# Kernel tuning notes

Measured on AMD Instinct MI355X. Metric: run time of the kernel, lower is better.

## Reference

```python
import jax, jax.numpy as jnp
import numpy as np
from jax import lax

B, A, H, W = 4, 9, 128, 128
FEAT_STRIDE = 16
PRE_NMS_TOPN = 4000
POST_NMS_TOPN = 1000
NMS_THRESH = 0.7
IM_SIZE = 2048.0


def _generate_anchors(base_size=16, ratios=(0.5, 1.0, 2.0), scales=(8.0, 16.0, 32.0)):
    base = np.array([1.0, 1.0, base_size, base_size], dtype=np.float32) - 1.0

    def whctrs(a):
        w = a[2] - a[0] + 1.0
        h = a[3] - a[1] + 1.0
        return w, h, a[0] + 0.5 * (w - 1.0), a[1] + 0.5 * (h - 1.0)

    def mk(ws, hs, xc, yc):
        ws = ws[:, None]
        hs = hs[:, None]
        return np.hstack([xc - 0.5 * (ws - 1.0), yc - 0.5 * (hs - 1.0),
                          xc + 0.5 * (ws - 1.0), yc + 0.5 * (hs - 1.0)])

    w, h, xc, yc = whctrs(base)
    size = w * h
    r = np.array(ratios, dtype=np.float32)
    ws = np.round(np.sqrt(size / r))
    hs = np.round(ws * r)
    ratio_anchors = mk(ws, hs, xc, yc)
    out = []
    s = np.array(scales, dtype=np.float32)
    for a in ratio_anchors:
        w2, h2, xc2, yc2 = whctrs(a)
        out.append(mk(w2 * s, h2 * s, xc2, yc2))
    return np.vstack(out).astype(np.float32)  # [A, 4]


ANCHORS = jnp.asarray(_generate_anchors(FEAT_STRIDE))


def setup_inputs() -> dict:
    key = jax.random.key(0)
    k1, k2 = jax.random.split(key)
    scores = jax.random.normal(k1, (B, 2 * A, H, W), dtype=jnp.float32)
    bbox_deltas = jax.random.normal(k2, (B, 4 * A, H, W), dtype=jnp.float32) * 0.5
    im_info = jnp.tile(jnp.array([IM_SIZE, IM_SIZE, 1.0], dtype=jnp.float32), (B, 1))
    valid_range = jnp.tile(jnp.array([0.0, 10000.0], dtype=jnp.float32), (B, 1))
    return {"scores": scores, "bbox_deltas": bbox_deltas, "im_info": im_info,
            "valid_range": valid_range}


def _bbox_transform_inv(anchors, deltas):
    # anchors [N,4] broadcast against deltas [B,N,4]
    w = anchors[..., 2] - anchors[..., 0] + 1.0
    h = anchors[..., 3] - anchors[..., 1] + 1.0
    cx = anchors[..., 0] + 0.5 * w
    cy = anchors[..., 1] + 0.5 * h
    dx, dy, dw, dh = deltas[..., 0], deltas[..., 1], deltas[..., 2], deltas[..., 3]
    pcx = dx * w + cx
    pcy = dy * h + cy
    pw = jnp.exp(dw) * w
    ph = jnp.exp(dh) * h
    return jnp.stack([pcx - 0.5 * pw, pcy - 0.5 * ph,
                      pcx + 0.5 * pw, pcy + 0.5 * ph], axis=-1)


def _clip_boxes(boxes, im_hw):
    # boxes [B,N,4]; im_hw [B,2] = (height, width)
    boxes = jnp.maximum(boxes, 0.0)
    hmax = im_hw[:, 0][:, None] - 1.0
    wmax = im_hw[:, 1][:, None] - 1.0
    return jnp.stack([jnp.minimum(boxes[..., 0], wmax),
                      jnp.minimum(boxes[..., 1], hmax),
                      jnp.minimum(boxes[..., 2], wmax),
                      jnp.minimum(boxes[..., 3], hmax)], axis=-1)


def _iou_matrix(boxes):
    # boxes [N,4], +1 pixel convention (matches gpu_nms)
    x1, y1, x2, y2 = boxes[:, 0], boxes[:, 1], boxes[:, 2], boxes[:, 3]
    areas = (x2 - x1 + 1.0) * (y2 - y1 + 1.0)
    iw = jnp.maximum(jnp.minimum(x2[:, None], x2[None, :]) - jnp.maximum(x1[:, None], x1[None, :]) + 1.0, 0.0)
    ih = jnp.maximum(jnp.minimum(y2[:, None], y2[None, :]) - jnp.maximum(y1[:, None], y1[None, :]) + 1.0, 0.0)
    inter = iw * ih
    return inter / (areas[:, None] + areas[None, :] - inter)


def _nms_single(proposals, scores_flat):
    # proposals [KA,4], scores_flat [KA] -> [POST,4] zero-padded, score-ordered
    _, order = lax.top_k(scores_flat, PRE_NMS_TOPN)
    boxes = proposals[order]  # [PRE,4] sorted by descending score
    sup_mat = lax.stop_gradient(_iou_matrix(boxes) > NMS_THRESH)
    idxs = jnp.arange(PRE_NMS_TOPN)

    def body(i, supp):
        row = sup_mat[i] & (idxs > i)
        return jnp.where(supp[i], supp, supp | row)

    supp = lax.fori_loop(0, PRE_NMS_TOPN, body, jnp.zeros(PRE_NMS_TOPN, dtype=bool))
    keep = ~supp
    # stable argsort puts kept indices first, preserving score order
    kidx = jnp.argsort(jnp.where(keep, 0, 1), stable=True)[:POST_NMS_TOPN]
    valid = (jnp.arange(POST_NMS_TOPN) < keep.sum()).astype(boxes.dtype)
    return boxes[kidx] * valid[:, None]


def reference(scores, bbox_deltas, im_info, valid_range):
    fg = scores[:, A:, :, :]                      # [B,A,Hf,Wf] objectness scores
    Bc, _, Hf, Wf = fg.shape
    # anchor grid: [K,4] shifts + [A,4] base anchors -> [K*A,4]
    sx = jnp.arange(Wf, dtype=jnp.float32) * FEAT_STRIDE
    sy = jnp.arange(Hf, dtype=jnp.float32) * FEAT_STRIDE
    gx, gy = jnp.meshgrid(sx, sy)                 # [Hf,Wf] (xy indexing like np.meshgrid)
    shifts = jnp.stack([gx.ravel(), gy.ravel(), gx.ravel(), gy.ravel()], axis=1)  # [K,4]
    anchors = (ANCHORS[None, :, :] + shifts[:, None, :]).reshape(-1, 4)           # [K*A,4]

    deltas = bbox_deltas.transpose(0, 2, 3, 1).reshape(Bc, -1, 4)  # [B,K*A,4]
    sc = fg.transpose(0, 2, 3, 1).reshape(Bc, -1)                   # [B,K*A]

    proposals = _bbox_transform_inv(anchors[None, :, :], deltas)
    proposals = _clip_boxes(proposals, im_info[:, :2])

    # filter_proposal_by_range: area = w*h (no +1), score -> -1 if out of range
    widths = proposals[..., 2] - proposals[..., 0]
    heights = proposals[..., 3] - proposals[..., 1]
    area = widths * heights
    min_a = (valid_range[:, 0] ** 2)[:, None]
    max_a = (valid_range[:, 1] ** 2)[:, None]
    sc = jnp.where((area < min_a) | (area > max_a), -1.0, sc)

    out_boxes = jax.vmap(_nms_single)(proposals, sc)  # [B,POST,4]
    batch_col = jnp.broadcast_to(
        jnp.arange(Bc, dtype=out_boxes.dtype)[:, None, None], (Bc, POST_NMS_TOPN, 1))
    return jnp.concatenate([batch_col, out_boxes], axis=-1)  # [B,POST,5]
```

## Files before the change

### kernel.cpp

```cpp
#include <hip/hip_runtime.h>
#include <cmath>

#define WD 128
#define HT 128
#define HW 16384
#define NB 4
#define NA 9
#define NPB (NA*HW)
#define TOPN 4000
#define POSTN 1000
#define CANDCAP 8192
#define MROWS 4096
#define RST 4160
#define NTILE 63
#define TRI (NTILE*(NTILE+1)/2)
#define NREP 4
#define PBLK 576
#define NBLK 42

typedef unsigned long long u64;
typedef unsigned int u32;

struct Anchors { float v[36]; };

static void gen_anchors(float* out) {
    double base[4] = {0.0, 0.0, 15.0, 15.0};
    const double ratios[3] = {0.5, 1.0, 2.0};
    const double scales[3] = {8.0, 16.0, 32.0};
    double w = base[2] - base[0] + 1.0;
    double h = base[3] - base[1] + 1.0;
    double xc = base[0] + 0.5 * (w - 1.0);
    double yc = base[1] + 0.5 * (h - 1.0);
    double size = w * h;
    double ra[3][4];
    for (int r = 0; r < 3; ++r) {
        double ws = nearbyint(sqrt(size / ratios[r]));
        double hs = nearbyint(ws * ratios[r]);
        ra[r][0] = xc - 0.5 * (ws - 1.0);
        ra[r][1] = yc - 0.5 * (hs - 1.0);
        ra[r][2] = xc + 0.5 * (ws - 1.0);
        ra[r][3] = yc + 0.5 * (hs - 1.0);
    }
    int k = 0;
    for (int r = 0; r < 3; ++r) {
        double w2 = ra[r][2] - ra[r][0] + 1.0;
        double h2 = ra[r][3] - ra[r][1] + 1.0;
        double x2c = ra[r][0] + 0.5 * (w2 - 1.0);
        double y2c = ra[r][1] + 0.5 * (h2 - 1.0);
        for (int s = 0; s < 3; ++s) {
            double ws = w2 * scales[s], hs = h2 * scales[s];
            out[k*4+0] = (float)(x2c - 0.5 * (ws - 1.0));
            out[k*4+1] = (float)(y2c - 0.5 * (hs - 1.0));
            out[k*4+2] = (float)(x2c + 0.5 * (ws - 1.0));
            out[k*4+3] = (float)(y2c + 0.5 * (hs - 1.0));
            ++k;
        }
    }
}

__device__ __forceinline__ u32 sortable_key(float sc) {
    u32 sb = __float_as_uint(sc);
    return sb ^ ((sb & 0x80000000u) ? 0xFFFFFFFFu : 0x80000000u);
}

__device__ __forceinline__ u64 readlane64(u64 v, int l) {
    u32 lo = (u32)__builtin_amdgcn_readlane((int)(u32)v, l);
    u32 hi = (u32)__builtin_amdgcn_readlane((int)(u32)(v >> 32), l);
    return ((u64)hi << 32) | lo;
}

__device__ __forceinline__ u64 wave_or64_dpp(u64 v) {
    u32 lo = (u32)v, hi = (u32)(v >> 32);
#define DPPOR(x, ctrl) x |= (u32)__builtin_amdgcn_update_dpp(0, (int)(x), ctrl, 0xf, 0xf, false)
    DPPOR(lo, 0x111); DPPOR(lo, 0x112); DPPOR(lo, 0x114); DPPOR(lo, 0x118);
    DPPOR(lo, 0x142); DPPOR(lo, 0x143);
    DPPOR(hi, 0x111); DPPOR(hi, 0x112); DPPOR(hi, 0x114); DPPOR(hi, 0x118);
    DPPOR(hi, 0x142); DPPOR(hi, 0x143);
#undef DPPOR
    u32 rlo = (u32)__builtin_amdgcn_readlane((int)lo, 63);
    u32 rhi = (u32)__builtin_amdgcn_readlane((int)hi, 63);
    return ((u64)rhi << 32) | rlo;
}

__device__ __forceinline__ float4 decode_box(const float* __restrict__ deltas,
                                             const float* __restrict__ im_info,
                                             const Anchors& A, int b, int a, int p)
{
#pragma clang fp contract(off)
    int hh = p >> 7;
    int ww = p & 127;
    float sx = (float)(ww * 16);
    float sy = (float)(hh * 16);
    float ax1 = A.v[a*4+0] + sx;
    float ay1 = A.v[a*4+1] + sy;
    float ax2 = A.v[a*4+2] + sx;
    float ay2 = A.v[a*4+3] + sy;
    const float* dbase = deltas + ((size_t)(b*36 + a*4))*HW + p;
    float dx = dbase[0];
    float dy = dbase[HW];
    float dw = dbase[2*HW];
    float dh = dbase[3*HW];
    float aw = ax2 - ax1 + 1.0f;
    float ah = ay2 - ay1 + 1.0f;
    float cx = ax1 + 0.5f*aw;
    float cy = ay1 + 0.5f*ah;
    float pcx = dx*aw + cx;
    float pcy = dy*ah + cy;
    float ew = (float)exp((double)dw);
    float eh = (float)exp((double)dh);
    float pw = ew * aw;
    float ph = eh * ah;
    float x1 = pcx - 0.5f*pw;
    float y1 = pcy - 0.5f*ph;
    float x2 = pcx + 0.5f*pw;
    float y2 = pcy + 0.5f*ph;
    float hmax = im_info[b*3+0] - 1.0f;
    float wmax = im_info[b*3+1] - 1.0f;
    x1 = fmaxf(x1, 0.0f); y1 = fmaxf(y1, 0.0f);
    x2 = fmaxf(x2, 0.0f); y2 = fmaxf(y2, 0.0f);
    x1 = fminf(x1, wmax); y1 = fminf(y1, hmax);
    x2 = fminf(x2, wmax); y2 = fminf(y2, hmax);
    return make_float4(x1, y1, x2, y2);
}

__global__ void k_props(const float* __restrict__ scores,
                        const float* __restrict__ deltas,
                        const float* __restrict__ im_info,
                        const float* __restrict__ valid_range,
                        Anchors A,
                        u32* __restrict__ fkeys,
                        u32* __restrict__ coarseH)
{
#pragma clang fp contract(off)
    __shared__ u32 lh[256];
    int tid = threadIdx.x;
    lh[tid] = 0;
    __syncthreads();

    int n = blockIdx.x * 256 + tid;
    int b = n / NPB;
    int r = n - b*NPB;
    int a = r / HW;
    int p = r - a*HW;

    float4 bx = decode_box(deltas, im_info, A, b, a, p);
    float sc = scores[((size_t)(b*18 + 9 + a))*HW + p];
    float area = (bx.z - bx.x) * (bx.w - bx.y);
    float v0 = valid_range[b*2+0], v1 = valid_range[b*2+1];
    if (area < v0*v0 || area > v1*v1) sc = -1.0f;

    u32 key = sortable_key(sc);
    fkeys[n] = key;
    atomicAdd(&lh[key >> 24], 1u);
    __syncthreads();

    u32 v = lh[tid];
    if (v) {
        int rep = blockIdx.x & (NREP-1);
        atomicAdd(&coarseH[((size_t)rep*NB + b)*256 + tid], v);
    }
}

__global__ void k_findA(const u32* __restrict__ coarseH,
                        int* __restrict__ cstar, u32* __restrict__ cabove)
{
    __shared__ u32 sfx[256];
    int b = blockIdx.x, t = threadIdx.x;
    u32 s = 0;
    for (int rr = 0; rr < NREP; ++rr) s += coarseH[((size_t)rr*NB + b)*256 + t];
    sfx[t] = s;
    __syncthreads();
    for (int d = 1; d < 256; d <<= 1) {
        u32 add = (t + d < 256) ? sfx[t + d] : 0u;
        __syncthreads();
        sfx[t] += add;
        __syncthreads();
    }
    u32 mine = sfx[t];
    u32 nxt  = (t < 255) ? sfx[t+1] : 0u;
    if (mine >= TOPN && (t == 255 || nxt < TOPN)) { cstar[b] = t; cabove[b] = nxt; }
}

__global__ void k_fineHist(const u32* __restrict__ fkeys,
                           const int* __restrict__ cstar,
                           u32* __restrict__ fineH)
{
    int n = blockIdx.x * 256 + threadIdx.x;
    int b = n / NPB;
    u32 key = fkeys[n];
    if ((int)(key >> 24) == cstar[b]) {
        int rep = blockIdx.x & (NREP-1);
        atomicAdd(&fineH[((size_t)rep*NB + b)*256 + ((key >> 16) & 255u)], 1u);
    }
}

__global__ void k_findB(const u32* __restrict__ fineH,
                        const int* __restrict__ cstar, const u32* __restrict__ cabove,
                        u32* __restrict__ thresh16)
{
    __shared__ u32 sfx[256];
    int b = blockIdx.x, t = threadIdx.x;
    u32 s = 0;
    for (int rr = 0; rr < NREP; ++rr) s += fineH[((size_t)rr*NB + b)*256 + t];
    sfx[t] = s;
    __syncthreads();
    for (int d = 1; d < 256; d <<= 1) {
        u32 add = (t + d < 256) ? sfx[t + d] : 0u;
        __syncthreads();
        sfx[t] += add;
        __syncthreads();
    }
    u32 ca   = cabove[b];
    u32 mine = ca + sfx[t];
    u32 nxt  = (t < 255) ? (ca + sfx[t+1]) : ca;
    if (mine >= TOPN && (t == 255 || nxt < TOPN))
        thresh16[b] = ((u32)cstar[b] << 8) | (u32)t;
}

__global__ void k_count(const u32* __restrict__ fkeys,
                        const u32* __restrict__ thresh16,
                        u32* __restrict__ bcnt)
{
    int n = blockIdx.x * 256 + threadIdx.x;
    int b = n / NPB;
    bool cond = (fkeys[n] >> 16) >= thresh16[b];
    u64 m = __ballot(cond);
    __shared__ u32 wc[4];
    int wave = threadIdx.x >> 6;
    if ((threadIdx.x & 63) == 0) wc[wave] = (u32)__popcll(m);
    __syncthreads();
    if (threadIdx.x == 0) bcnt[blockIdx.x] = wc[0] + wc[1] + wc[2] + wc[3];
}

__global__ void k_scanblk(const u32* __restrict__ bcnt,
                          u32* __restrict__ bbase, u32* __restrict__ ccnt)
{
    __shared__ u32 s[PBLK];
    int b = blockIdx.x, t = threadIdx.x;
    u32 v = bcnt[b*PBLK + t];
    s[t] = v;
    __syncthreads();
    for (int d = 1; d < PBLK; d <<= 1) {
        u32 add = (t >= d) ? s[t-d] : 0;
        __syncthreads();
        s[t] += add;
        __syncthreads();
    }
    bbase[b*PBLK + t] = s[t] - v;
    if (t == PBLK-1) ccnt[b] = s[t];
}

__global__ void k_emit(const u32* __restrict__ fkeys,
                       const u32* __restrict__ thresh16,
                       const u32* __restrict__ bbase,
                       u64* __restrict__ cand)
{
    int n = blockIdx.x * 256 + threadIdx.x;
    int b = n / NPB;
    int r = n - b*NPB;
    int a = r / HW;
    int p = r - a*HW;
    u32 key = fkeys[n];
    bool cond = (key >> 16) >= thresh16[b];
    u64 m = __ballot(cond);
    int lane = threadIdx.x & 63;
    int wave = threadIdx.x >> 6;
    __shared__ u32 wb[4];
    if (lane == 0) wb[wave] = (u32)__popcll(m);
    __syncthreads();
    if (cond) {
        u32 wbase = 0;
        for (int wv = 0; wv < wave; ++wv) wbase += wb[wv];
        u32 off = (u32)__popcll(m & ((1ull << lane) - 1ull));
        u32 pos = bbase[blockIdx.x] + wbase + off;
        if (pos < CANDCAP) {
            u32 t = (u32)(p*NA + a);
            cand[(size_t)b*CANDCAP + pos] = ((u64)key << 32) | (u32)(~t);
        }
    }
}

__global__ void k_rank2(const u64* __restrict__ cand, const u32* __restrict__ ccnt,
                        const float* __restrict__ deltas,
                        const float* __restrict__ im_info,
                        Anchors A,
                        float4* __restrict__ topk)
{
    __shared__ u64 kk[CANDCAP];
    __shared__ u32 ps[256];
    int b = blockIdx.y;
    u32 N = ccnt[b]; if (N > CANDCAP) N = CANDCAP;
    int tid = threadIdx.x;
    if ((u32)(blockIdx.x * 64) >= N) return;
    for (u32 i = tid; i < N; i += 256) kk[i] = cand[(size_t)b*CANDCAP + i];
    __syncthreads();
    int kl = tid & 63, seg = tid >> 6;
    u32 ki = (u32)(blockIdx.x * 64 + kl);
    u64 mykey = (ki < N) ? kk[ki] : ~0ull;
    u32 segN = (N + 3) >> 2;
    u32 s0 = seg * segN;
    u32 s1 = s0 + segN; if (s1 > N) s1 = N;
    u32 pr = 0;
    u32 i = s0;
    for (; i + 16 <= s1; i += 16) {
        u64 v0 = kk[i+0],  v1 = kk[i+1],  v2 = kk[i+2],  v3 = kk[i+3];
        u64 v4 = kk[i+4],  v5 = kk[i+5],  v6 = kk[i+6],  v7 = kk[i+7];
        u64 v8 = kk[i+8],  v9 = kk[i+9],  va = kk[i+10], vb = kk[i+11];
        u64 vc = kk[i+12], vd = kk[i+13], ve = kk[i+14], vf = kk[i+15];
        pr += (v0 > mykey) + (v1 > mykey) + (v2 > mykey) + (v3 > mykey);
        pr += (v4 > mykey) + (v5 > mykey) + (v6 > mykey) + (v7 > mykey);
        pr += (v8 > mykey) + (v9 > mykey) + (va > mykey) + (vb > mykey);
        pr += (vc > mykey) + (vd > mykey) + (ve > mykey) + (vf > mykey);
    }
    for (; i < s1; ++i) pr += (kk[i] > mykey) ? 1u : 0u;
    ps[tid] = pr;
    __syncthreads();
    if (seg == 0 && ki < N) {
        u32 rank = ps[kl] + ps[kl+64] + ps[kl+128] + ps[kl+192];
        if (rank < TOPN) {
            u32 t = ~((u32)mykey);
            int a = (int)(t % 9u);
            int p = (int)(t / 9u);
            topk[(size_t)b*MROWS + rank] = decode_box(deltas, im_info, A, b, a, p);
        }
    }
}

__global__ void k_mask(const float4* __restrict__ topk, u64* __restrict__ masksT)
{
#pragma clang fp contract(off)
    int L = blockIdx.x;
    int b = blockIdx.y;
    int ti = (int)((2.0*NTILE + 1.0 -
                    sqrt((2.0*NTILE + 1.0)*(2.0*NTILE + 1.0) - 8.0*(double)L)) * 0.5);
    while ((ti+1)*NTILE - ((ti+1)*ti)/2 <= L) ++ti;
    while (ti*NTILE - (ti*(ti-1))/2 > L) --ti;
    int tj = ti + (L - (ti*NTILE - (ti*(ti-1))/2));

    int r = threadIdx.x;
    int i = ti*64 + r;
    __shared__ float4 cb[64];
    __shared__ float  ca[64];
    u64 word = 0;
    {
        int jj = tj*64 + r;
        float4 cbox = (jj < TOPN) ? topk[(size_t)b*MROWS + jj] : make_float4(0,0,0,0);
        cb[r] = cbox;
        ca[r] = (cbox.z - cbox.x + 1.0f) * (cbox.w - cbox.y + 1.0f);
        __syncthreads();
        if (i < TOPN) {
            float4 rb = topk[(size_t)b*MROWS + i];
            float rarea = (rb.z - rb.x + 1.0f) * (rb.w - rb.y + 1.0f);
            for (int q = 0; q < 64; ++q) {
                float4 cc = cb[q];
                float iw = fminf(rb.z, cc.z) - fmaxf(rb.x, cc.x) + 1.0f;
                float ih = fminf(rb.w, cc.w) - fmaxf(rb.y, cc.y) + 1.0f;
                iw = fmaxf(iw, 0.0f); ih = fmaxf(ih, 0.0f);
                float inter = iw * ih;
                float uni = (rarea + ca[q]) - inter;
                float iou = inter / uni;
                if (iou > 0.7f) word |= (1ULL << q);
            }
            int nvalid = TOPN - tj*64;
            if (nvalid < 64) word &= ((1ULL << nvalid) - 1ULL);
            if (ti == tj) {
                u64 cm = (r == 63) ? ~0ULL : ((1ULL << (r + 1)) - 1ULL);
                word &= ~cm;
            }
        }
    }
    masksT[((size_t)(b*64 + tj))*RST + i] = word;
}

#define NMS_PLOAD(cc) { \
    int cm = ((cc) > 62) ? 62 : (cc); \
    const u64* colp = mb + (size_t)cm*RST; \
    _Pragma("unroll") \
    for (int k = 0; k < NBLK; ++k) \
        if (k <= cm) pf[k] = colp[(size_t)k*64 + lane]; \
}

#define NMS_PSTORE(cc) { \
    int cm = ((cc) > 62) ? 62 : (cc); \
    int wmax = (cm < NBLK-1) ? cm+1 : NBLK; \
    _Pragma("unroll") \
    for (int k = 0; k < NBLK; ++k) \
        if (k < wmax) colbuf[k*64 + lane] = pf[k]; \
}

__global__ __launch_bounds__(64, 1) void k_nms(const u64* __restrict__ masksT,
                      const float4* __restrict__ topk,
                      float* __restrict__ out)
{
    int b = blockIdx.x;
    int lane = threadIdx.x;

    __shared__ u64 colbuf[NBLK*64];
    __shared__ u32 kmexp[64][64];
    __shared__ u64 kmw[64];

    kmw[lane] = 0ull;
#pragma unroll
    for (int k = 0; k < 64; ++k) kmexp[k][lane] = 0u;

    {
        float* ob = out + (size_t)b*POSTN*5;
        for (int e = lane; e < POSTN*5; e += 64)
            ob[e] = ((e % 5) == 0) ? (float)b : 0.0f;
    }

    const u64* mb = masksT + (size_t)b*64*RST;

    u64 pf[NBLK];
    NMS_PLOAD(0)
    NMS_PSTORE(0)
    NMS_PLOAD(1)

    int kcnt = 0;
    for (int c = 0; c < 63; ++c) {
        u64 acc = 0;
        int kmax = (c < NBLK) ? c : NBLK;
#pragma unroll 8
        for (int k = 0; k < kmax; ++k) {
            u32 mk = kmexp[k][lane];
            u64 v = colbuf[k*64 + lane];
            acc |= v & (((u64)mk << 32) | mk);
        }
        for (int k = NBLK; k < c; ++k) {
            u32 mk = kmexp[k][lane];
            u64 v = mb[(size_t)c*RST + (size_t)k*64 + lane];
            acc |= v & (((u64)mk << 32) | mk);
        }
        u64 w = wave_or64_dpp(acc);
        u64 D = (c < NBLK) ? colbuf[c*64 + lane]
                           : mb[(size_t)c*RST + (size_t)c*64 + lane];
#pragma unroll
        for (int r = 0; r < 64; ++r) {
            u64 dr = readlane64(D, r);
            u64 t;
            asm("s_lshr_b64 %[t], %[w], %[rr]\n\t"
                "s_and_b64 %[t], %[t], 1\n\t"
                "s_cselect_b64 %[t], 0, %[d]\n\t"
                "s_or_b64 %[w], %[w], %[t]"
                : [w]"+s"(w), [t]"=&s"(t)
                : [d]"s"(dr), [rr]"i"(r)
                : "scc");
        }
        u64 kmask = ~w & ((c < 62) ? ~0ull : 0xFFFFFFFFull);
        kcnt += __popcll(kmask);
        if (lane == 0) kmw[c] = kmask;
        kmexp[c][lane] = ((u32)((kmask >> lane) & 1ull)) ? ~0u : 0u;

        if (kcnt >= POSTN || c == 62) break;
        NMS_PSTORE(c+1)
        NMS_PLOAD(c+2)
    }

    u64 keepw = kmw[lane];
    int cnt = __popcll(keepw);
    int pre = cnt;
    for (int d = 1; d < 64; d <<= 1) {
        int t = __shfl_up(pre, d);
        if (lane >= d) pre += t;
    }
    int excl = pre - cnt;
    asm volatile("s_waitcnt vmcnt(0)" ::: "memory");
    u64 wv = keepw; int rk = excl;
    while (wv) {
        int bpos = __ffsll((unsigned long long)wv) - 1;
        wv &= wv - 1;
        if (rk < POSTN) {
            int i = lane*64 + bpos;
            float4 bx = topk[(size_t)b*MROWS + i];
            float* o = out + ((size_t)b*POSTN + rk)*5;
            o[1] = bx.x; o[2] = bx.y; o[3] = bx.z; o[4] = bx.w;
        }
        ++rk;
    }
}

extern "C" void kernel_launch(void* const* d_in, const int* in_sizes, int n_in,
                              void* d_out, int out_size, void* d_ws, size_t ws_size,
                              hipStream_t stream)
{
    const float* scores  = (const float*)d_in[0];
    const float* deltas  = (const float*)d_in[1];
    const float* im_info = (const float*)d_in[2];
    const float* vrange  = (const float*)d_in[3];
    float* out = (float*)d_out;

    char* ws = (char*)d_ws;
    size_t off = 0;
    auto alloc = [&](size_t bytes) -> void* {
        void* ptr = ws + off;
        off += (bytes + 255) & ~(size_t)255;
        return ptr;
    };
    u32*   fkeys   = (u32*)   alloc((size_t)NB*NPB*sizeof(u32));
    u64*   cand    = (u64*)   alloc((size_t)NB*CANDCAP*sizeof(u64));
    float4* topk   = (float4*)alloc((size_t)NB*MROWS*sizeof(float4));
    u64*   masksT  = (u64*)   alloc((size_t)NB*64*RST*sizeof(u64));
    u32*   bcnt    = (u32*)   alloc((size_t)NB*PBLK*sizeof(u32));
    u32*   bbase   = (u32*)   alloc((size_t)NB*PBLK*sizeof(u32));
    u32*   coarseH = (u32*)   alloc((size_t)NREP*NB*256*sizeof(u32));
    u32*   fineH   = (u32*)   alloc((size_t)NREP*NB*256*sizeof(u32));
    u32*   ccnt    = (u32*)   alloc(256);
    int*   cstar   = (int*)   alloc(256);
    u32*   cabove  = (u32*)   alloc(256);
    u32*   thresh16= (u32*)   alloc(256);

    Anchors A;
    gen_anchors(A.v);

    size_t zbytes = (char*)fineH + (size_t)NREP*NB*256*sizeof(u32) - (char*)coarseH;
    hipMemsetAsync(coarseH, 0, zbytes, stream);

    int total = NB*NPB;
    int blocks = (total + 255)/256;
    k_props<<<blocks, 256, 0, stream>>>(scores, deltas, im_info, vrange, A, fkeys, coarseH);
    k_findA<<<NB, 256, 0, stream>>>(coarseH, cstar, cabove);
    k_fineHist<<<blocks, 256, 0, stream>>>(fkeys, cstar, fineH);
    k_findB<<<NB, 256, 0, stream>>>(fineH, cstar, cabove, thresh16);
    k_count<<<blocks, 256, 0, stream>>>(fkeys, thresh16, bcnt);
    k_scanblk<<<NB, PBLK, 0, stream>>>(bcnt, bbase, ccnt);
    k_emit<<<blocks, 256, 0, stream>>>(fkeys, thresh16, bbase, cand);
    dim3 rgrid(CANDCAP/64, NB);
    k_rank2<<<rgrid, 256, 0, stream>>>(cand, ccnt, deltas, im_info, A, topk);
    dim3 mgrid(TRI, NB);
    k_mask<<<mgrid, 64, 0, stream>>>(topk, masksT);
    k_nms<<<NB, 64, 0, stream>>>(masksT, topk, out);
}
```

Baseline: 143.5 us.

## Replace two-pass radix threshold with single 12-bit histogram and atomic compaction

The two-level 8-bit radix select (coarse histogram, find, fine histogram pass, find) becomes a single 4096-bin 12-bit histogram built in k_props. The count and scan kernels are replaced by wave-level atomic append into 32 replicated candidate buckets. This drops three full passes over the keys and several launches. In exchange the coarser threshold admits more candidates, each bucket is capped at 1024 entries with the total capped at 8192, and k_props gains a larger shared histogram and more global atomics.

```diff
diff --git a/kernel.cpp b/kernel.cpp
--- a/kernel.cpp
+++ b/kernel.cpp
@@ -10,12 +10,15 @@
 #define TOPN 4000
 #define POSTN 1000
 #define CANDCAP 8192
+#define REPCAP 1024
+#define NREPL 32
 #define MROWS 4096
 #define RST 4160
 #define NTILE 63
 #define TRI (NTILE*(NTILE+1)/2)
 #define NREP 4
 #define PBLK 576
+#define NBINS 4096
 #define NBLK 42
 
 typedef unsigned long long u64;
@@ -129,12 +132,13 @@
                         const float* __restrict__ valid_range,
                         Anchors A,
                         u32* __restrict__ fkeys,
-                        u32* __restrict__ coarseH)
+                        u32* __restrict__ hist12)
 {
 #pragma clang fp contract(off)
-    __shared__ u32 lh[256];
+    __shared__ u32 lh[NBINS];
     int tid = threadIdx.x;
-    lh[tid] = 0;
+#pragma unroll
+    for (int i = 0; i < NBINS/256; ++i) lh[tid + i*256] = 0;
     __syncthreads();
 
     int n = blockIdx.x * 256 + tid;
@@ -151,136 +155,78 @@
 
     u32 key = sortable_key(sc);
     fkeys[n] = key;
-    atomicAdd(&lh[key >> 24], 1u);
-    __syncthreads();
-
-    u32 v = lh[tid];
-    if (v) {
-        int rep = blockIdx.x & (NREP-1);
-        atomicAdd(&coarseH[((size_t)rep*NB + b)*256 + tid], v);
-    }
-}
-
-__global__ void k_findA(const u32* __restrict__ coarseH,
-                        int* __restrict__ cstar, u32* __restrict__ cabove)
-{
-    __shared__ u32 sfx[256];
+    atomicAdd(&lh[key >> 20], 1u);
+    __syncthreads();
+
+    int rep = blockIdx.x & (NREP-1);
+    u32* gh = hist12 + ((size_t)rep*NB + b)*NBINS;
+#pragma unroll
+    for (int i = 0; i < NBINS/256; ++i) {
+        u32 v = lh[tid + i*256];
+        if (v) atomicAdd(&gh[tid + i*256], v);
+    }
+}
+
+__global__ void k_findT(const u32* __restrict__ hist12, u32* __restrict__ thresh12)
+{
+    __shared__ u32 sfx[1024];
     int b = blockIdx.x, t = threadIdx.x;
-    u32 s = 0;
-    for (int rr = 0; rr < NREP; ++rr) s += coarseH[((size_t)rr*NB + b)*256 + t];
-    sfx[t] = s;
-    __syncthreads();
-    for (int d = 1; d < 256; d <<= 1) {
-        u32 add = (t + d < 256) ? sfx[t + d] : 0u;
+    u32 bin0 = 0, bin1 = 0, bin2 = 0, bin3 = 0;
+    for (int rr = 0; rr < NREP; ++rr) {
+        const u32* h = hist12 + ((size_t)rr*NB + b)*NBINS + t*4;
+        bin0 += h[0]; bin1 += h[1]; bin2 += h[2]; bin3 += h[3];
+    }
+    u32 s4 = bin0 + bin1 + bin2 + bin3;
+    sfx[t] = s4;
+    __syncthreads();
+    for (int d = 1; d < 1024; d <<= 1) {
+        u32 add = (t + d < 1024) ? sfx[t + d] : 0u;
         __syncthreads();
         sfx[t] += add;
         __syncthreads();
     }
-    u32 mine = sfx[t];
-    u32 nxt  = (t < 255) ? sfx[t+1] : 0u;
-    if (mine >= TOPN && (t == 255 || nxt < TOPN)) { cstar[b] = t; cabove[b] = nxt; }
-}
-
-__global__ void k_fineHist(const u32* __restrict__ fkeys,
-                           const int* __restrict__ cstar,
-                           u32* __restrict__ fineH)
-{
-    int n = blockIdx.x * 256 + threadIdx.x;
-    int b = n / NPB;
-    u32 key = fkeys[n];
-    if ((int)(key >> 24) == cstar[b]) {
-        int rep = blockIdx.x & (NREP-1);
-        atomicAdd(&fineH[((size_t)rep*NB + b)*256 + ((key >> 16) & 255u)], 1u);
-    }
-}
-
-__global__ void k_findB(const u32* __restrict__ fineH,
-                        const int* __restrict__ cstar, const u32* __restrict__ cabove,
-                        u32* __restrict__ thresh16)
-{
-    __shared__ u32 sfx[256];
-    int b = blockIdx.x, t = threadIdx.x;
-    u32 s = 0;
-    for (int rr = 0; rr < NREP; ++rr) s += fineH[((size_t)rr*NB + b)*256 + t];
-    sfx[t] = s;
-    __syncthreads();
-    for (int d = 1; d < 256; d <<= 1) {
-        u32 add = (t + d < 256) ? sfx[t + d] : 0u;
-        __syncthreads();
-        sfx[t] += add;
-        __syncthreads();
-    }
-    u32 ca   = cabove[b];
-    u32 mine = ca + sfx[t];
-    u32 nxt  = (t < 255) ? (ca + sfx[t+1]) : ca;
-    if (mine >= TOPN && (t == 255 || nxt < TOPN))
-        thresh16[b] = ((u32)cstar[b] << 8) | (u32)t;
-}
-
-__global__ void k_count(const u32* __restrict__ fkeys,
-                        const u32* __restrict__ thresh16,
-                        u32* __restrict__ bcnt)
-{
-    int n = blockIdx.x * 256 + threadIdx.x;
-    int b = n / NPB;
-    bool cond = (fkeys[n] >> 16) >= thresh16[b];
-    u64 m = __ballot(cond);
-    __shared__ u32 wc[4];
-    int wave = threadIdx.x >> 6;
-    if ((threadIdx.x & 63) == 0) wc[wave] = (u32)__popcll(m);
-    __syncthreads();
-    if (threadIdx.x == 0) bcnt[blockIdx.x] = wc[0] + wc[1] + wc[2] + wc[3];
-}
-
-__global__ void k_scanblk(const u32* __restrict__ bcnt,
-                          u32* __restrict__ bbase, u32* __restrict__ ccnt)
-{
-    __shared__ u32 s[PBLK];
-    int b = blockIdx.x, t = threadIdx.x;
-    u32 v = bcnt[b*PBLK + t];
-    s[t] = v;
-    __syncthreads();
-    for (int d = 1; d < PBLK; d <<= 1) {
-        u32 add = (t >= d) ? s[t-d] : 0;
-        __syncthreads();
-        s[t] += add;
-        __syncthreads();
-    }
-    bbase[b*PBLK + t] = s[t] - v;
-    if (t == PBLK-1) ccnt[b] = s[t];
+    u32 above = (t < 1023) ? sfx[t+1] : 0u;
+    u32 c3 = bin3 + above;
+    u32 c2 = bin2 + c3;
+    u32 c1 = bin1 + c2;
+    u32 c0 = bin0 + c1;
+    if (c3 >= TOPN && above < TOPN) thresh12[b] = (u32)(t*4 + 3);
+    if (c2 >= TOPN && c3    < TOPN) thresh12[b] = (u32)(t*4 + 2);
+    if (c1 >= TOPN && c2    < TOPN) thresh12[b] = (u32)(t*4 + 1);
+    if (c0 >= TOPN && c1    < TOPN) thresh12[b] = (u32)(t*4 + 0);
 }
 
 __global__ void k_emit(const u32* __restrict__ fkeys,
-                       const u32* __restrict__ thresh16,
-                       const u32* __restrict__ bbase,
+                       const u32* __restrict__ thresh12,
+                       u32* __restrict__ ccntRep,
                        u64* __restrict__ cand)
 {
-    int n = blockIdx.x * 256 + threadIdx.x;
+    int tid = threadIdx.x;
+    int n = blockIdx.x * 256 + tid;
     int b = n / NPB;
     int r = n - b*NPB;
     int a = r / HW;
     int p = r - a*HW;
     u32 key = fkeys[n];
-    bool cond = (key >> 16) >= thresh16[b];
+    bool cond = (key >> 20) >= thresh12[b];
     u64 m = __ballot(cond);
-    int lane = threadIdx.x & 63;
-    int wave = threadIdx.x >> 6;
-    __shared__ u32 wb[4];
-    if (lane == 0) wb[wave] = (u32)__popcll(m);
-    __syncthreads();
+    int lane = tid & 63;
+    int rep = blockIdx.x & (NREPL-1);
     if (cond) {
-        u32 wbase = 0;
-        for (int wv = 0; wv < wave; ++wv) wbase += wb[wv];
-        u32 off = (u32)__popcll(m & ((1ull << lane) - 1ull));
-        u32 pos = bbase[blockIdx.x] + wbase + off;
-        if (pos < CANDCAP) {
+        int leader = __ffsll((unsigned long long)m) - 1;
+        u32 base = 0;
+        if (lane == leader)
+            base = atomicAdd(&ccntRep[(b*NREPL + rep)*16], (u32)__popcll(m));
+        base = (u32)__shfl((int)base, leader);
+        u32 pos = base + (u32)__popcll(m & ((1ull << lane) - 1ull));
+        if (pos < REPCAP) {
             u32 t = (u32)(p*NA + a);
-            cand[(size_t)b*CANDCAP + pos] = ((u64)key << 32) | (u32)(~t);
-        }
-    }
-}
-
-__global__ void k_rank2(const u64* __restrict__ cand, const u32* __restrict__ ccnt,
+            cand[((size_t)b*NREPL + rep)*REPCAP + pos] = ((u64)key << 32) | (u32)(~t);
+        }
+    }
+}
+
+__global__ void k_rank2(const u64* __restrict__ cand, const u32* __restrict__ ccntRep,
                         const float* __restrict__ deltas,
                         const float* __restrict__ im_info,
                         Anchors A,
@@ -288,11 +234,31 @@
 {
     __shared__ u64 kk[CANDCAP];
     __shared__ u32 ps[256];
+    __shared__ u32 rcnt[32];
+    __shared__ u32 roff[33];
     int b = blockIdx.y;
-    u32 N = ccnt[b]; if (N > CANDCAP) N = CANDCAP;
     int tid = threadIdx.x;
+    if (tid < 32) {
+        u32 c = ccntRep[(b*NREPL + tid)*16];
+        rcnt[tid] = (c > REPCAP) ? REPCAP : c;
+    }
+    __syncthreads();
+    if (tid == 0) {
+        u32 acc = 0;
+        for (int i = 0; i < 32; ++i) { roff[i] = acc; acc += rcnt[i]; }
+        roff[32] = (acc > CANDCAP) ? CANDCAP : acc;
+    }
+    __syncthreads();
+    u32 N = roff[32];
     if ((u32)(blockIdx.x * 64) >= N) return;
-    for (u32 i = tid; i < N; i += 256) kk[i] = cand[(size_t)b*CANDCAP + i];
+    for (int rr = 0; rr < 32; ++rr) {
+        u32 len = rcnt[rr], base = roff[rr];
+        const u64* src = cand + ((size_t)b*NREPL + rr)*REPCAP;
+        for (u32 i = tid; i < len; i += 256) {
+            u32 g = base + i;
+            if (g < CANDCAP) kk[g] = src[i];
+        }
+    }
     __syncthreads();
     int kl = tid & 63, seg = tid >> 6;
     u32 ki = (u32)(blockIdx.x * 64 + kl);
@@ -497,35 +463,26 @@
         return ptr;
     };
     u32*   fkeys   = (u32*)   alloc((size_t)NB*NPB*sizeof(u32));
-    u64*   cand    = (u64*)   alloc((size_t)NB*CANDCAP*sizeof(u64));
+    u64*   cand    = (u64*)   alloc((size_t)NB*NREPL*REPCAP*sizeof(u64));
     float4* topk   = (float4*)alloc((size_t)NB*MROWS*sizeof(float4));
     u64*   masksT  = (u64*)   alloc((size_t)NB*64*RST*sizeof(u64));
-    u32*   bcnt    = (u32*)   alloc((size_t)NB*PBLK*sizeof(u32));
-    u32*   bbase   = (u32*)   alloc((size_t)NB*PBLK*sizeof(u32));
-    u32*   coarseH = (u32*)   alloc((size_t)NREP*NB*256*sizeof(u32));
-    u32*   fineH   = (u32*)   alloc((size_t)NREP*NB*256*sizeof(u32));
-    u32*   ccnt    = (u32*)   alloc(256);
-    int*   cstar   = (int*)   alloc(256);
-    u32*   cabove  = (u32*)   alloc(256);
-    u32*   thresh16= (u32*)   alloc(256);
+    u32*   hist12  = (u32*)   alloc((size_t)NREP*NB*NBINS*sizeof(u32));
+    u32*   ccntRep = (u32*)   alloc((size_t)NB*NREPL*16*sizeof(u32));
+    u32*   thresh12= (u32*)   alloc(256);
 
     Anchors A;
     gen_anchors(A.v);
 
-    size_t zbytes = (char*)fineH + (size_t)NREP*NB*256*sizeof(u32) - (char*)coarseH;
-    hipMemsetAsync(coarseH, 0, zbytes, stream);
+    size_t zbytes = (char*)ccntRep + (size_t)NB*NREPL*16*sizeof(u32) - (char*)hist12;
+    hipMemsetAsync(hist12, 0, zbytes, stream);
 
     int total = NB*NPB;
     int blocks = (total + 255)/256;
-    k_props<<<blocks, 256, 0, stream>>>(scores, deltas, im_info, vrange, A, fkeys, coarseH);
-    k_findA<<<NB, 256, 0, stream>>>(coarseH, cstar, cabove);
-    k_fineHist<<<blocks, 256, 0, stream>>>(fkeys, cstar, fineH);
-    k_findB<<<NB, 256, 0, stream>>>(fineH, cstar, cabove, thresh16);
-    k_count<<<blocks, 256, 0, stream>>>(fkeys, thresh16, bcnt);
-    k_scanblk<<<NB, PBLK, 0, stream>>>(bcnt, bbase, ccnt);
-    k_emit<<<blocks, 256, 0, stream>>>(fkeys, thresh16, bbase, cand);
+    k_props<<<blocks, 256, 0, stream>>>(scores, deltas, im_info, vrange, A, fkeys, hist12);
+    k_findT<<<NB, 1024, 0, stream>>>(hist12, thresh12);
+    k_emit<<<blocks, 256, 0, stream>>>(fkeys, thresh12, ccntRep, cand);
     dim3 rgrid(CANDCAP/64, NB);
-    k_rank2<<<rgrid, 256, 0, stream>>>(cand, ccnt, deltas, im_info, A, topk);
+    k_rank2<<<rgrid, 256, 0, stream>>>(cand, ccntRep, deltas, im_info, A, topk);
     dim3 mgrid(TRI, NB);
     k_mask<<<mgrid, 64, 0, stream>>>(topk, masksT);
     k_nms<<<NB, 64, 0, stream>>>(masksT, topk, out);
```

Result: faster. 134.3 us (-6.4%).
